# Performance work log

Measured on AMD Instinct MI355X. Metric: run time of the kernel, lower is better.

Reference implementation:

```python
import jax, jax.numpy as jnp
import numpy as np

N = 20000   # nodes
E = 320000  # edges
C = 64      # channel multiplicity
NB = 8      # bessel basis size
NA = 4      # node attribute (species) dim
L_DIMS = (1, 3, 5)  # 2l+1 for l=0,1,2
SH = 9      # total spherical-harmonic dim
OFFS = (0, 1, 4, 9)


def setup_inputs() -> dict:
    key = jax.random.key(0)
    ks = jax.random.split(key, 11)
    s = lambda k, shape: jax.random.normal(k, shape, dtype=jnp.float32)
    return {
        "length": jax.random.uniform(ks[0], (E, NB), dtype=jnp.float32),
        "node_features": s(ks[1], (N, C)),
        "node_attributes": s(ks[2], (N, NA)),
        "edge_attributes": s(ks[3], (E, SH)),
        "W1": s(ks[4], (NB, 64)),
        "W2": s(ks[5], (64, 64)),
        "W3": s(ks[6], (64, 64)),
        "W4": s(ks[7], (64, 3 * C)),
        "Wl": s(ks[8], (3, C, C)),
        "Wsc": s(ks[9], (NA, C, C)),
        "edge_index": jax.random.randint(ks[10], (2, E), 0, N, dtype=jnp.int32),
    }


def reference(length, node_features, node_attributes, edge_attributes, W1, W2, W3, W4, Wl, Wsc, edge_index):
    sender, receiver = edge_index[0], edge_index[1]
    silu = jax.nn.silu
    # e3nn FullyConnectedNet: x @ W / sqrt(fan_in), silu between layers, no act on last
    h = silu(length @ W1 * np.float32(1.0 / np.sqrt(NB)))
    h = silu(h @ W2 * np.float32(0.125))
    h = silu(h @ W3 * np.float32(0.125))
    w = (h @ W4 * np.float32(0.125)).reshape(E, 3, C)  # per-edge TP weights [E,3,C]
    # weighted tensor product: scalar node feats x sh (0e x le -> le, uvu)
    wx = w * node_features[sender][:, None, :]          # [E,3,C]
    parts = []
    for l in range(3):
        Y = edge_attributes[:, OFFS[l]:OFFS[l + 1]]     # [E, 2l+1]
        parts.append((wx[:, l, :, None] * Y[:, None, :]).reshape(E, C * L_DIMS[l]))
    mij = jnp.concatenate(parts, axis=1)                # [E, C*9]
    # scatter_sum into receivers
    msg = jax.ops.segment_sum(mij, receiver, num_segments=N)  # [N, C*9]
    # e3nn Linear: per-l channel mix, 1/sqrt(fan_in) norm
    out_blocks = []
    o = 0
    for l in range(3):
        d = L_DIMS[l]
        blk = msg[:, o:o + C * d].reshape(N, C, d)
        out_blocks.append(jnp.einsum('num,uv->nvm', blk, Wl[l]) * np.float32(1.0 / np.sqrt(C)))
        o += C * d
    message = jnp.concatenate(out_blocks, axis=2)       # reshape_irreps -> [N, C, 9]
    # FullyConnectedTensorProduct(attr 0e, feat 0e) -> only 0e output has paths
    sc0 = jnp.einsum('na,nu,auw->nw', node_attributes, node_features, Wsc) * np.float32(1.0 / np.sqrt(NA * C))
    sc = jnp.concatenate([sc0, jnp.zeros((N, C * (SH - 1)), dtype=sc0.dtype)], axis=1)  # [N, C*9]
    return (message, sc)
```

## Files before the change

kernel.cpp:

```cpp
#include <hip/hip_runtime.h>
#include <hip/hip_fp16.h>

#define N_NODES 20000
#define N_EDGES 320000
#define MSG_ROW 576
#define MSG_OFF 11520000
#define SCAN_BS 256
#define NBLK_SCAN ((N_NODES + SCAN_BS - 1) / SCAN_BS)
#define NPAD 20032
#define MT_S (NPAD * 64)

typedef _Float16 f16;
typedef _Float16 f16x4 __attribute__((ext_vector_type(4)));
typedef _Float16 f16x8 __attribute__((ext_vector_type(8)));
typedef float f32x4 __attribute__((ext_vector_type(4)));

#define OFF_WLT  22528
#define OFF_WSCT 34816
#define WIMG_HALF 51200
#define WIMG_BYTES 102400
#define WIMG_BLOCKS 200

#define OFF_WT4 0
#define OFF_W1T 24576
#define OFF_WT2 28672
#define OFF_WT3 36864
#define OFF_H0  45056
#define OFF_HT  53248
#define LDS_TOTAL 69632
#define OFF_WXT 0

__device__ __forceinline__ float silu_f(float x) {
    return x * __builtin_amdgcn_rcpf(1.0f + __expf(-x));
}


__global__ __launch_bounds__(256)
void pre_kernel(const float* __restrict__ W1, const float* __restrict__ W2,
                const float* __restrict__ W3, const float* __restrict__ W4,
                const float* __restrict__ Wl, const float* __restrict__ Wsc,
                f16* __restrict__ img,
                const int* __restrict__ eidx, int* __restrict__ counts) {
    const int b = blockIdx.x;
    if (b >= WIMG_BLOCKS) {
        const int e = (b - WIMG_BLOCKS) * 256 + threadIdx.x;
        if (e < N_EDGES) atomicAdd(&counts[eidx[N_EDGES + e]], 1);
        return;
    }
    const int p = b * 256 + threadIdx.x;
    float v;
    if (p < 12288) {
        const int m = p >> 6, rem = p & 63, g = rem >> 3, j = rem & 7;
        const int k = ((g ^ (m & 7)) << 3) | j;
        v = W4[k * 192 + m];
    } else if (p < 14336) {
        const int q = p - 12288;
        const int m = q >> 5, rem = q & 31, g = rem >> 3, j = rem & 7;
        const int k = ((g ^ (m & 3)) << 3) | j;
        v = (k < 8) ? W1[k * 64 + m] : 0.f;
    } else if (p < 18432) {
        const int q = p - 14336;
        const int m = q >> 6, rem = q & 63, g = rem >> 3, j = rem & 7;
        const int k = ((g ^ (m & 7)) << 3) | j;
        v = W2[k * 64 + m];
    } else if (p < 22528) {
        const int q = p - 18432;
        const int m = q >> 6, rem = q & 63, g = rem >> 3, j = rem & 7;
        const int k = ((g ^ (m & 7)) << 3) | j;
        v = W3[k * 64 + m];
    } else if (p < OFF_WSCT) {
        const int q = p - OFF_WLT;
        const int l = q >> 12, r = q & 4095, vv = r >> 6, u = r & 63;
        v = Wl[(l * 64 + u) * 64 + vv];
    } else {
        const int q = p - OFF_WSCT;
        const int ww = q >> 8, kk = q & 255, a = kk >> 6, u = kk & 63;
        v = Wsc[(a * 64 + u) * 64 + ww];
    }
    img[p] = (f16)v;
}


__global__ __launch_bounds__(SCAN_BS)
void scan1_kernel(const int* __restrict__ counts, int* __restrict__ offs,
                  int* __restrict__ bsum) {
    __shared__ int sm[SCAN_BS];
    const int tid = threadIdx.x;
    const int i = blockIdx.x * SCAN_BS + tid;
    const int v = (i < N_NODES) ? counts[i] : 0;
    sm[tid] = v;
    __syncthreads();
#pragma unroll
    for (int off = 1; off < SCAN_BS; off <<= 1) {
        const int t = (tid >= off) ? sm[tid - off] : 0;
        __syncthreads();
        sm[tid] += t;
        __syncthreads();
    }
    if (i < N_NODES) offs[i] = sm[tid] - v;
    if (tid == SCAN_BS - 1) bsum[blockIdx.x] = sm[tid];
}

__global__ __launch_bounds__(SCAN_BS)
void scan3_kernel(int* __restrict__ offs, const int* __restrict__ bsum,
                  int* __restrict__ cursor) {
    __shared__ int bs[NBLK_SCAN];
    const int tid = threadIdx.x;
    if (tid < NBLK_SCAN) bs[tid] = bsum[tid];
    __syncthreads();
    int bbase = 0;
    for (int j = 0; j < blockIdx.x; ++j) bbase += bs[j];
    const int i = blockIdx.x * SCAN_BS + tid;
    if (i < N_NODES) {
        const int o = offs[i] + bbase;
        offs[i] = o;
        cursor[i] = o;
    }
    if (blockIdx.x == NBLK_SCAN - 1 && tid == SCAN_BS - 1)
        offs[N_NODES] = bbase + bs[NBLK_SCAN - 1];
}


__global__ __launch_bounds__(512, 4)
void edge_mlp_mfma(const float* __restrict__ length,
                   const float* __restrict__ nf,
                   const int*   __restrict__ eidx,
                   int* __restrict__ cursor,
                   int* __restrict__ order,
                   const f16*   __restrict__ wimg,
                   f16* __restrict__ wx)
{
    __shared__ __align__(16) char s[LDS_TOTAL];
    __shared__ int sendS[128];
    __shared__ int rankS[128];

    const int tid = threadIdx.x;
    const int ebase = blockIdx.x << 7;

    {
        const uint4* src = (const uint4*)wimg;
        uint4* dst = (uint4*)s;
#pragma unroll
        for (int i = 0; i < 6; ++i) {
            const int c = i * 512 + tid;
            if (c < 2816) dst[c] = src[c];
        }
    }
    if (tid < 128) {
        const int e = tid;
        const int eg = ebase + e;
        const float4 q0 = *(const float4*)&length[(size_t)eg * 8];
        const float4 q1 = *(const float4*)&length[(size_t)eg * 8 + 4];
        f16x8 h;
        h[0] = (f16)q0.x; h[1] = (f16)q0.y; h[2] = (f16)q0.z; h[3] = (f16)q0.w;
        h[4] = (f16)q1.x; h[5] = (f16)q1.y; h[6] = (f16)q1.z; h[7] = (f16)q1.w;
        *(f16x8*)(s + OFF_H0 + e * 64 + ((0 ^ (e & 3)) << 4)) = h;
        sendS[e] = eidx[eg];
        const int rcv = eidx[N_EDGES + eg];
        const int pos = atomicAdd(&cursor[rcv], 1);
        order[pos] = eg;
        rankS[e] = pos;
    } else {
        const int idx = tid - 128;
        const int e = idx / 3, gz = 1 + idx - (idx / 3) * 3;
        uint4 z; z.x = 0; z.y = 0; z.z = 0; z.w = 0;
        *(uint4*)(s + OFF_H0 + e * 64 + ((gz ^ (e & 3)) << 4)) = z;
    }
    __syncthreads();

    const int lane = tid & 63, w = tid >> 6;
    const int eh = w >> 2, wm = w & 3;
    const int lm = lane & 15, lg = lane >> 4;
    const int mrow = wm * 16 + lm;
    const int r0 = lg << 2;
    const int eloc0 = eh << 6;

    const f32x4 zacc = {0.f, 0.f, 0.f, 0.f};
    f32x4 acc[4];

    {
        const f16x8 a = *(const f16x8*)(s + OFF_W1T + mrow * 64 + ((lg ^ (mrow & 3)) << 4));
#pragma unroll
        for (int nt = 0; nt < 4; ++nt) {
            const int e = eloc0 + nt * 16 + lm;
            const f16x8 b = *(const f16x8*)(s + OFF_H0 + e * 64 + ((lg ^ (e & 3)) << 4));
            acc[nt] = __builtin_amdgcn_mfma_f32_16x16x32_f16(a, b, zacc, 0, 0, 0);
        }
    }
    {
        const int c = wm * 16 + r0;
#pragma unroll
        for (int nt = 0; nt < 4; ++nt) {
            const int e = eloc0 + nt * 16 + lm;
            f16x4 pk;
            pk[0] = (f16)silu_f(acc[nt][0] * 0.35355339059f);
            pk[1] = (f16)silu_f(acc[nt][1] * 0.35355339059f);
            pk[2] = (f16)silu_f(acc[nt][2] * 0.35355339059f);
            pk[3] = (f16)silu_f(acc[nt][3] * 0.35355339059f);
            *(f16x4*)(s + OFF_HT + e * 128 + (((c >> 3) ^ (e & 7)) << 4) + ((c & 7) << 1)) = pk;
        }
    }
    __syncthreads();

#pragma unroll
    for (int nt = 0; nt < 4; ++nt) acc[nt] = zacc;
#pragma unroll
    for (int kh = 0; kh < 2; ++kh) {
        const int g = (kh << 2) + lg;
        const f16x8 a = *(const f16x8*)(s + OFF_WT2 + mrow * 128 + ((g ^ (mrow & 7)) << 4));
#pragma unroll
        for (int nt = 0; nt < 4; ++nt) {
            const int e = eloc0 + nt * 16 + lm;
            const f16x8 b = *(const f16x8*)(s + OFF_HT + e * 128 + ((g ^ (e & 7)) << 4));
            acc[nt] = __builtin_amdgcn_mfma_f32_16x16x32_f16(a, b, acc[nt], 0, 0, 0);
        }
    }
    __syncthreads();
    {
        const int c = wm * 16 + r0;
#pragma unroll
        for (int nt = 0; nt < 4; ++nt) {
            const int e = eloc0 + nt * 16 + lm;
            f16x4 pk;
            pk[0] = (f16)silu_f(acc[nt][0] * 0.125f);
            pk[1] = (f16)silu_f(acc[nt][1] * 0.125f);
            pk[2] = (f16)silu_f(acc[nt][2] * 0.125f);
            pk[3] = (f16)silu_f(acc[nt][3] * 0.125f);
            *(f16x4*)(s + OFF_HT + e * 128 + (((c >> 3) ^ (e & 7)) << 4) + ((c & 7) << 1)) = pk;
        }
    }
    __syncthreads();

#pragma unroll
    for (int nt = 0; nt < 4; ++nt) acc[nt] = zacc;
#pragma unroll
    for (int kh = 0; kh < 2; ++kh) {
        const int g = (kh << 2) + lg;
        const f16x8 a = *(const f16x8*)(s + OFF_WT3 + mrow * 128 + ((g ^ (mrow & 7)) << 4));
#pragma unroll
        for (int nt = 0; nt < 4; ++nt) {
            const int e = eloc0 + nt * 16 + lm;
            const f16x8 b = *(const f16x8*)(s + OFF_HT + e * 128 + ((g ^ (e & 7)) << 4));
            acc[nt] = __builtin_amdgcn_mfma_f32_16x16x32_f16(a, b, acc[nt], 0, 0, 0);
        }
    }
    __syncthreads();
    {
        const int c = wm * 16 + r0;
#pragma unroll
        for (int nt = 0; nt < 4; ++nt) {
            const int e = eloc0 + nt * 16 + lm;
            f16x4 pk;
            pk[0] = (f16)silu_f(acc[nt][0] * 0.125f);
            pk[1] = (f16)silu_f(acc[nt][1] * 0.125f);
            pk[2] = (f16)silu_f(acc[nt][2] * 0.125f);
            pk[3] = (f16)silu_f(acc[nt][3] * 0.125f);
            *(f16x4*)(s + OFF_HT + e * 128 + (((c >> 3) ^ (e & 7)) << 4) + ((c & 7) << 1)) = pk;
        }
    }
    __syncthreads();

    f32x4 acc4[3][4];
#pragma unroll
    for (int p = 0; p < 3; ++p)
#pragma unroll
        for (int nt = 0; nt < 4; ++nt) acc4[p][nt] = zacc;
#pragma unroll
    for (int kh = 0; kh < 2; ++kh) {
        const int g = (kh << 2) + lg;
        f16x8 ap[3];
#pragma unroll
        for (int p = 0; p < 3; ++p) {
            const int m4 = p * 64 + mrow;
            ap[p] = *(const f16x8*)(s + OFF_WT4 + m4 * 128 + ((g ^ (m4 & 7)) << 4));
        }
#pragma unroll
        for (int nt = 0; nt < 4; ++nt) {
            const int e = eloc0 + nt * 16 + lm;
            const f16x8 b = *(const f16x8*)(s + OFF_HT + e * 128 + ((g ^ (e & 7)) << 4));
#pragma unroll
            for (int p = 0; p < 3; ++p)
                acc4[p][nt] = __builtin_amdgcn_mfma_f32_16x16x32_f16(ap[p], b, acc4[p][nt], 0, 0, 0);
        }
    }
    __syncthreads();

#pragma unroll
    for (int nt = 0; nt < 4; ++nt) {
        const int e = eloc0 + nt * 16 + lm;
        const int snd = sendS[e];
        const float4 nf4 = *(const float4*)&nf[(size_t)snd * 64 + wm * 16 + r0];
#pragma unroll
        for (int p = 0; p < 3; ++p) {
            const int c = p * 64 + wm * 16 + r0;
            f16x4 pk;
            pk[0] = (f16)(acc4[p][nt][0] * 0.125f * nf4.x);
            pk[1] = (f16)(acc4[p][nt][1] * 0.125f * nf4.y);
            pk[2] = (f16)(acc4[p][nt][2] * 0.125f * nf4.z);
            pk[3] = (f16)(acc4[p][nt][3] * 0.125f * nf4.w);
            *(f16x4*)(s + OFF_WXT + e * 384 + (((c >> 3) ^ (e & 7)) << 4) + ((c & 7) << 1)) = pk;
        }
    }
    __syncthreads();

#pragma unroll
    for (int it = 0; it < 6; ++it) {
        const int chunk = it * 512 + tid;
        const int e = chunk / 24, g = chunk - e * 24;
        const uint4 v = *(const uint4*)(s + OFF_WXT + e * 384 + ((g ^ (e & 7)) << 4));
        *(uint4*)((char*)wx + (size_t)rankS[e] * 384 + g * 16) = v;
    }
}


__global__ __launch_bounds__(256, 8)
void gather_kernel(const __half* __restrict__ wx,
                   const float* __restrict__ ea,
                   const int* __restrict__ offs,
                   const int* __restrict__ order,
                   f16* __restrict__ mT)
{
    const int tid = threadIdx.x;
    const int wid = tid >> 6;
    const int v   = tid & 63;
    const int n   = (blockIdx.x << 2) + wid;
    const int beg = offs[n];
    const int end = offs[n + 1];

    float a0 = 0.f, a1[3] = {0.f, 0.f, 0.f}, a2[5] = {0.f, 0.f, 0.f, 0.f, 0.f};
    int k = beg;
    for (; k + 2 <= end; k += 2) {
        const int eA = __builtin_amdgcn_readfirstlane(order[k]);
        const int eB = __builtin_amdgcn_readfirstlane(order[k + 1]);
        const __half* wrA = wx + (size_t)k * 192;
        const __half* wrB = wx + (size_t)(k + 1) * 192;
        const float xA0 = __half2float(wrA[v]);
        const float xA1 = __half2float(wrA[64 + v]);
        const float xA2 = __half2float(wrA[128 + v]);
        const float xB0 = __half2float(wrB[v]);
        const float xB1 = __half2float(wrB[64 + v]);
        const float xB2 = __half2float(wrB[128 + v]);
        const float* yA = ea + (size_t)eA * 9;
        const float* yB = ea + (size_t)eB * 9;
        a0 += xA0 * yA[0] + xB0 * yB[0];
#pragma unroll
        for (int m = 0; m < 3; ++m) a1[m] += xA1 * yA[1 + m] + xB1 * yB[1 + m];
#pragma unroll
        for (int m = 0; m < 5; ++m) a2[m] += xA2 * yA[4 + m] + xB2 * yB[4 + m];
    }
    if (k < end) {
        const int e = __builtin_amdgcn_readfirstlane(order[k]);
        const __half* wr = wx + (size_t)k * 192;
        const float x0 = __half2float(wr[v]);
        const float x1 = __half2float(wr[64 + v]);
        const float x2 = __half2float(wr[128 + v]);
        const float* y = ea + (size_t)e * 9;
        a0 += x0 * y[0];
#pragma unroll
        for (int m = 0; m < 3; ++m) a1[m] += x1 * y[1 + m];
#pragma unroll
        for (int m = 0; m < 5; ++m) a2[m] += x2 * y[4 + m];
    }

    f16* base = mT + (size_t)n * 64 + v;
    base[0] = (f16)a0;
#pragma unroll
    for (int m = 0; m < 3; ++m) base[(size_t)(1 + m) * MT_S] = (f16)a1[m];
#pragma unroll
    for (int m = 0; m < 5; ++m) base[(size_t)(4 + m) * MT_S] = (f16)a2[m];
}


__global__ __launch_bounds__(256, 2)
void node_mfma(const f16* __restrict__ wimg,
               const f16* __restrict__ mT,
               const float* __restrict__ nf,
               const float* __restrict__ na,
               float* __restrict__ out)
{
    __shared__ __align__(16) f16  mst[9 * 16 * 64];
    __shared__ __align__(16) f16  nft[16 * 64];
    __shared__ __align__(16) float nas[256];
    __shared__ __align__(16) float outb[16 * 580];

    const int tid = threadIdx.x;
    const int lane = tid & 63, w = tid >> 6;
    const int lm = lane & 15, lg = lane >> 4;
    const int r0 = lg << 2;
    const int n0 = blockIdx.x << 6;

    const f16* wlT  = wimg + OFF_WLT;
    const f16* wscT = wimg + OFF_WSCT;
    f16x8 wl[3][2];
#pragma unroll
    for (int l = 0; l < 3; ++l)
#pragma unroll
        for (int kk = 0; kk < 2; ++kk)
            wl[l][kk] = *(const f16x8*)(wlT + ((l << 6) + (w << 4) + lm) * 64 + (kk << 5) + (lg << 3));
    f16x8 wsc[8];
#pragma unroll
    for (int kg = 0; kg < 8; ++kg)
        wsc[kg] = *(const f16x8*)(wscT + ((w << 4) + lm) * 256 + (kg << 5) + (lg << 3));

    {
        const int n = n0 + (tid >> 2);
        nas[tid] = (n < N_NODES) ? na[(size_t)n * 4 + (tid & 3)] : 0.f;
    }

    const f32x4 zacc = {0.f, 0.f, 0.f, 0.f};

    for (int nt = 0; nt < 4; ++nt) {
        const int ng = n0 + (nt << 4);
        __syncthreads();

#pragma unroll
        for (int it = 0; it < 5; ++it) {
            const int c = it * 256 + tid;
            if (c < 1152) {
                const int m = c >> 7, rem = c & 127, r = rem >> 3, g = rem & 7;
                const uint4 v = *(const uint4*)(mT + (size_t)m * MT_S + (size_t)(ng + r) * 64 + (g << 3));
                *(uint4*)(&mst[m * 1024 + r * 64 + ((g ^ (r & 7)) << 3)]) = v;
            }
        }
        {
            const int r = tid >> 4, c4 = (tid & 15) << 2;
            const int n = ng + r;
            float4 v4;
            if (n < N_NODES) v4 = *(const float4*)&nf[(size_t)n * 64 + c4];
            else { v4.x = 0.f; v4.y = 0.f; v4.z = 0.f; v4.w = 0.f; }
            f16x4 h;
            h[0] = (f16)v4.x; h[1] = (f16)v4.y; h[2] = (f16)v4.z; h[3] = (f16)v4.w;
            const int g = c4 >> 3;
            *(f16x4*)&nft[r * 64 + ((g ^ (r & 7)) << 3) + (c4 & 7)] = h;
        }
        __syncthreads();

#pragma unroll
        for (int m = 0; m < 9; ++m) {
            const int l = (m == 0) ? 0 : ((m < 4) ? 1 : 2);
            f32x4 acc = zacc;
#pragma unroll
            for (int kk = 0; kk < 2; ++kk) {
                const int g = (kk << 2) + lg;
                const f16x8 b = *(const f16x8*)&mst[m * 1024 + lm * 64 + ((g ^ (lm & 7)) << 3)];
                acc = __builtin_amdgcn_mfma_f32_16x16x32_f16(wl[l][kk], b, acc, 0, 0, 0);
            }
#pragma unroll
            for (int i = 0; i < 4; ++i)
                outb[lm * 580 + ((w << 4) + r0 + i) * 9 + m] = acc[i] * 0.125f;
        }
        __syncthreads();

#pragma unroll
        for (int it = 0; it < 9; ++it) {
            const int c = it * 256 + tid;
            const int r = c / 144, q = c - r * 144;
            const int n = ng + r;
            if (n < N_NODES) {
                const float4 v = *(const float4*)&outb[r * 580 + (q << 2)];
                *(float4*)&out[(size_t)n * 576 + (q << 2)] = v;
            }
        }
        __syncthreads();

        {
            const float4 na4 = *(const float4*)&nas[((nt << 4) + lm) << 2];
            const float* nap = (const float*)&na4;
            f32x4 sacc = zacc;
#pragma unroll
            for (int kg = 0; kg < 8; ++kg) {
                const int g = ((kg & 1) << 2) + lg;
                f16x8 q = *(const f16x8*)&nft[lm * 64 + ((g ^ (lm & 7)) << 3)];
                const f16 sa = (f16)nap[kg >> 1];
                q = q * sa;
                sacc = __builtin_amdgcn_mfma_f32_16x16x32_f16(wsc[kg], q, sacc, 0, 0, 0);
            }
#pragma unroll
            for (int i = 0; i < 4; ++i)
                outb[lm * 580 + (w << 4) + r0 + i] = sacc[i] * 0.0625f;
        }
        __syncthreads();

        {
            const int r = tid >> 4, q = tid & 15;
            const int n = ng + r;
            if (n < N_NODES)
                *(float4*)&out[(size_t)MSG_OFF + (size_t)n * 576 + (q << 2)] =
                    *(const float4*)&outb[r * 580 + (q << 2)];
        }
        float4 z4; z4.x = 0.f; z4.y = 0.f; z4.z = 0.f; z4.w = 0.f;
#pragma unroll
        for (int it = 0; it < 8; ++it) {
            const int c = it * 256 + tid;
            const int r = c >> 7, q = c & 127;
            const int n = ng + r;
            if (n < N_NODES)
                *(float4*)&out[(size_t)MSG_OFF + (size_t)n * 576 + 64 + (q << 2)] = z4;
        }
    }
}


__device__ __forceinline__ void layer_accum(const float* src, const float* __restrict__ W,
                                            float a2[4][4], int c0, int e0) {
#pragma unroll
    for (int i = 0; i < 4; ++i)
#pragma unroll
        for (int j = 0; j < 4; ++j) a2[i][j] = 0.f;
#pragma unroll 8
    for (int u = 0; u < 64; ++u) {
        const float4 h4 = *(const float4*)&src[(u << 6) + e0];
        const float4 w4 = *(const float4*)&W[(u << 6) + c0];
        const float hv[4] = {h4.x, h4.y, h4.z, h4.w};
        const float wv[4] = {w4.x, w4.y, w4.z, w4.w};
#pragma unroll
        for (int i = 0; i < 4; ++i)
#pragma unroll
            for (int j = 0; j < 4; ++j) a2[i][j] += wv[i] * hv[j];
    }
}

__device__ __forceinline__ void layer_store(float* dst, const float a2[4][4],
                                            float scale, int c0, int e0) {
#pragma unroll
    for (int i = 0; i < 4; ++i) {
        float4 v;
        v.x = silu_f(a2[i][0] * scale);
        v.y = silu_f(a2[i][1] * scale);
        v.z = silu_f(a2[i][2] * scale);
        v.w = silu_f(a2[i][3] * scale);
        *(float4*)&dst[((c0 + i) << 6) + e0] = v;
    }
}

__global__ __launch_bounds__(256, 4)
void edge_kernel_atomic(const float* __restrict__ length,
                        const float* __restrict__ nf,
                        const float* __restrict__ ea,
                        const float* __restrict__ W1,
                        const float* __restrict__ W2,
                        const float* __restrict__ W3,
                        const float* __restrict__ W4,
                        const int*   __restrict__ eidx,
                        float* __restrict__ msg)
{
    __shared__ float buf[4096];
    __shared__ float lenS[512];
    __shared__ float Ys[576];
    __shared__ int   sendS[64];
    __shared__ int   recvS[64];

    const int tid = threadIdx.x;
    const int tx = tid & 15;
    const int ty = tid >> 4;
    const int c0 = tx << 2;
    const int e0 = ty << 2;
    const int ebase = blockIdx.x << 6;

    for (int i = tid; i < 512; i += 256) {
        const int e = i >> 3, k = i & 7;
        lenS[(k << 6) + e] = length[((ebase + e) << 3) + k];
    }
    for (int i = tid; i < 576; i += 256) Ys[i] = ea[ebase * 9 + i];
    if (tid < 64) {
        sendS[tid] = eidx[ebase + tid];
        recvS[tid] = eidx[N_EDGES + ebase + tid];
    }
    __syncthreads();

    {
        float a2[4][4];
#pragma unroll
        for (int i = 0; i < 4; ++i)
#pragma unroll
            for (int j = 0; j < 4; ++j) a2[i][j] = 0.f;
#pragma unroll
        for (int k = 0; k < 8; ++k) {
            const float4 h4 = *(const float4*)&lenS[(k << 6) + e0];
            const float4 w4 = *(const float4*)&W1[(k << 6) + c0];
            const float hv[4] = {h4.x, h4.y, h4.z, h4.w};
            const float wv[4] = {w4.x, w4.y, w4.z, w4.w};
#pragma unroll
            for (int i = 0; i < 4; ++i)
#pragma unroll
                for (int j = 0; j < 4; ++j) a2[i][j] += wv[i] * hv[j];
        }
        layer_store(buf, a2, 0.35355339059327373f, c0, e0);
    }
    __syncthreads();
    {
        float a2[4][4];
        layer_accum(buf, W2, a2, c0, e0);
        __syncthreads();
        layer_store(buf, a2, 0.125f, c0, e0);
    }
    __syncthreads();
    {
        float a2[4][4];
        layer_accum(buf, W3, a2, c0, e0);
        __syncthreads();
        layer_store(buf, a2, 0.125f, c0, e0);
    }
    __syncthreads();

    float wacc[3][4][4];
#pragma unroll
    for (int l = 0; l < 3; ++l)
#pragma unroll
        for (int i = 0; i < 4; ++i)
#pragma unroll
            for (int j = 0; j < 4; ++j) wacc[l][i][j] = 0.f;
#pragma unroll 4
    for (int u = 0; u < 64; ++u) {
        const float4 h4 = *(const float4*)&buf[(u << 6) + e0];
        const float hv[4] = {h4.x, h4.y, h4.z, h4.w};
#pragma unroll
        for (int l = 0; l < 3; ++l) {
            const float4 w4 = *(const float4*)&W4[u * 192 + (l << 6) + c0];
            const float wv[4] = {w4.x, w4.y, w4.z, w4.w};
#pragma unroll
            for (int i = 0; i < 4; ++i)
#pragma unroll
                for (int j = 0; j < 4; ++j) wacc[l][i][j] += wv[i] * hv[j];
        }
    }

#pragma unroll
    for (int j = 0; j < 4; ++j) {
        const int e = e0 + j;
        const int snd = sendS[e];
        const int rcv = recvS[e];
        const float4 nf4 = *(const float4*)&nf[(snd << 6) + c0];
        const float nfv[4] = {nf4.x, nf4.y, nf4.z, nf4.w};
        float* mrow = msg + rcv * MSG_ROW;
        const float y0 = Ys[e * 9 + 0];
        float y1[3], y2[5];
#pragma unroll
        for (int m = 0; m < 3; ++m) y1[m] = Ys[e * 9 + 1 + m];
#pragma unroll
        for (int m = 0; m < 5; ++m) y2[m] = Ys[e * 9 + 4 + m];
#pragma unroll
        for (int i = 0; i < 4; ++i) {
            const int c = c0 + i;
            const float wx0 = wacc[0][i][j] * 0.125f * nfv[i];
            const float wx1 = wacc[1][i][j] * 0.125f * nfv[i];
            const float wx2 = wacc[2][i][j] * 0.125f * nfv[i];
            atomicAdd(&mrow[c], wx0 * y0);
#pragma unroll
            for (int m = 0; m < 3; ++m) atomicAdd(&mrow[64 + c * 3 + m], wx1 * y1[m]);
#pragma unroll
            for (int m = 0; m < 5; ++m) atomicAdd(&mrow[256 + c * 5 + m], wx2 * y2[m]);
        }
    }
}

__global__ __launch_bounds__(256, 4)
void node_kernel(const float* __restrict__ nf,
                 const float* __restrict__ na,
                 const float* __restrict__ Wl,
                 const float* __restrict__ Wsc,
                 float* __restrict__ out)
{
    __shared__ float ms[4][576];
    __shared__ float fs[4][64];
    const int tid = threadIdx.x;
    const int wid = tid >> 6;
    const int v   = tid & 63;
    const int n   = (blockIdx.x << 2) + wid;
    const float* msg = out + MSG_OFF;

#pragma unroll
    for (int j = 0; j < 9; ++j)
        ms[wid][(j << 6) + v] = msg[n * MSG_ROW + (j << 6) + v];
    fs[wid][v] = nf[(n << 6) + v];
    __syncthreads();

    float o9[9];
#pragma unroll
    for (int j = 0; j < 9; ++j) o9[j] = 0.f;
    const float* m0 = &ms[wid][0];
    const float* m1 = &ms[wid][64];
    const float* m2 = &ms[wid][256];

#pragma unroll 8
    for (int u = 0; u < 64; ++u) {
        const float w0 = Wl[(u << 6) + v];
        const float w1 = Wl[4096 + (u << 6) + v];
        const float w2 = Wl[8192 + (u << 6) + v];
        o9[0] += m0[u] * w0;
        o9[1] += m1[u * 3 + 0] * w1;
        o9[2] += m1[u * 3 + 1] * w1;
        o9[3] += m1[u * 3 + 2] * w1;
        o9[4] += m2[u * 5 + 0] * w2;
        o9[5] += m2[u * 5 + 1] * w2;
        o9[6] += m2[u * 5 + 2] * w2;
        o9[7] += m2[u * 5 + 3] * w2;
        o9[8] += m2[u * 5 + 4] * w2;
    }
#pragma unroll
    for (int j = 0; j < 9; ++j) out[n * MSG_ROW + v * 9 + j] = o9[j] * 0.125f;

    const float b0 = na[(n << 2) + 0];
    const float b1 = na[(n << 2) + 1];
    const float b2 = na[(n << 2) + 2];
    const float b3 = na[(n << 2) + 3];
    float sacc = 0.f;
#pragma unroll 8
    for (int u = 0; u < 64; ++u) {
        const float f = fs[wid][u];
        sacc += f * (b0 * Wsc[(u << 6) + v] + b1 * Wsc[4096 + (u << 6) + v] +
                     b2 * Wsc[8192 + (u << 6) + v] + b3 * Wsc[12288 + (u << 6) + v]);
    }
    float* scrow = out + MSG_OFF + n * MSG_ROW;
    scrow[v] = sacc * 0.0625f;
#pragma unroll
    for (int j = 1; j < 9; ++j) scrow[(j << 6) + v] = 0.f;
}

extern "C" void kernel_launch(void* const* d_in, const int* in_sizes, int n_in,
                              void* d_out, int out_size, void* d_ws, size_t ws_size,
                              hipStream_t stream) {
    const float* length = (const float*)d_in[0];
    const float* nfeat  = (const float*)d_in[1];
    const float* nattr  = (const float*)d_in[2];
    const float* eattr  = (const float*)d_in[3];
    const float* W1     = (const float*)d_in[4];
    const float* W2     = (const float*)d_in[5];
    const float* W3     = (const float*)d_in[6];
    const float* W4     = (const float*)d_in[7];
    const float* Wl     = (const float*)d_in[8];
    const float* Wsc    = (const float*)d_in[9];
    const int*   eidx   = (const int*)d_in[10];
    float* out = (float*)d_out;

    f16*    wimg   = (f16*)d_ws;
    __half* wx     = (__half*)((char*)d_ws + WIMG_BYTES);
    f16*    mT     = (f16*)((char*)d_ws + WIMG_BYTES + (size_t)N_EDGES * 192 * 2);
    int*   counts  = (int*)((char*)mT + (size_t)9 * MT_S * 2);
    int*   offsets = counts + N_NODES;
    int*   cursor  = offsets + N_NODES + 1;
    int*   order   = cursor + N_NODES;
    int*   bsum    = order + N_EDGES;
    const size_t need = WIMG_BYTES + (size_t)N_EDGES * 192 * 2 + (size_t)9 * MT_S * 2 +
                        (size_t)(N_NODES * 3 + 1 + N_EDGES + 128) * 4;

    if (ws_size >= need) {
        hipMemsetAsync(counts, 0, N_NODES * sizeof(int), stream);
        pre_kernel<<<WIMG_BLOCKS + N_EDGES / 256, 256, 0, stream>>>(W1, W2, W3, W4, Wl, Wsc,
                                                                    wimg, eidx, counts);
        scan1_kernel<<<NBLK_SCAN, SCAN_BS, 0, stream>>>(counts, offsets, bsum);
        scan3_kernel<<<NBLK_SCAN, SCAN_BS, 0, stream>>>(offsets, bsum, cursor);
        edge_mlp_mfma<<<N_EDGES / 128, 512, 0, stream>>>(length, nfeat, eidx, cursor, order,
                                                         wimg, (f16*)wx);
        gather_kernel<<<N_NODES / 4, 256, 0, stream>>>(wx, eattr, offsets, order, mT);
        node_mfma<<<NPAD / 64, 256, 0, stream>>>(wimg, mT, nfeat, nattr, out);
    } else {
        hipMemsetAsync(out + MSG_OFF, 0, (size_t)N_NODES * MSG_ROW * sizeof(float), stream);
        edge_kernel_atomic<<<N_EDGES / 64, 256, 0, stream>>>(length, nfeat, eattr,
                                                             W1, W2, W3, W4, eidx,
                                                             out + MSG_OFF);
        node_kernel<<<N_NODES / 4, 256, 0, stream>>>(nfeat, nattr, Wl, Wsc, out);
    }
}
```

Baseline: 146.4 us.

## Give each wave its own 16-edge strip to drop inter-layer barriers in edge MLP

```diff
diff --git a/kernel.cpp b/kernel.cpp
--- a/kernel.cpp
+++ b/kernel.cpp
@@ -169,146 +169,129 @@
     __syncthreads();
 
     const int lane = tid & 63, w = tid >> 6;
-    const int eh = w >> 2, wm = w & 3;
     const int lm = lane & 15, lg = lane >> 4;
-    const int mrow = wm * 16 + lm;
     const int r0 = lg << 2;
-    const int eloc0 = eh << 6;
+    const int e = (w << 4) + lm;
 
     const f32x4 zacc = {0.f, 0.f, 0.f, 0.f};
     f32x4 acc[4];
 
     {
-        const f16x8 a = *(const f16x8*)(s + OFF_W1T + mrow * 64 + ((lg ^ (mrow & 3)) << 4));
-#pragma unroll
-        for (int nt = 0; nt < 4; ++nt) {
-            const int e = eloc0 + nt * 16 + lm;
-            const f16x8 b = *(const f16x8*)(s + OFF_H0 + e * 64 + ((lg ^ (e & 3)) << 4));
-            acc[nt] = __builtin_amdgcn_mfma_f32_16x16x32_f16(a, b, zacc, 0, 0, 0);
-        }
-    }
-    {
-        const int c = wm * 16 + r0;
-#pragma unroll
-        for (int nt = 0; nt < 4; ++nt) {
-            const int e = eloc0 + nt * 16 + lm;
-            f16x4 pk;
-            pk[0] = (f16)silu_f(acc[nt][0] * 0.35355339059f);
-            pk[1] = (f16)silu_f(acc[nt][1] * 0.35355339059f);
-            pk[2] = (f16)silu_f(acc[nt][2] * 0.35355339059f);
-            pk[3] = (f16)silu_f(acc[nt][3] * 0.35355339059f);
-            *(f16x4*)(s + OFF_HT + e * 128 + (((c >> 3) ^ (e & 7)) << 4) + ((c & 7) << 1)) = pk;
-        }
-    }
-    __syncthreads();
-
-#pragma unroll
-    for (int nt = 0; nt < 4; ++nt) acc[nt] = zacc;
+        const f16x8 b = *(const f16x8*)(s + OFF_H0 + e * 64 + ((lg ^ (e & 3)) << 4));
+#pragma unroll
+        for (int ct = 0; ct < 4; ++ct) {
+            const int mrow = (ct << 4) + lm;
+            const f16x8 a = *(const f16x8*)(s + OFF_W1T + mrow * 64 + ((lg ^ (mrow & 3)) << 4));
+            acc[ct] = __builtin_amdgcn_mfma_f32_16x16x32_f16(a, b, zacc, 0, 0, 0);
+        }
+    }
+#pragma unroll
+    for (int ct = 0; ct < 4; ++ct) {
+        const int c = (ct << 4) + r0;
+        f16x4 pk;
+        pk[0] = (f16)silu_f(acc[ct][0] * 0.35355339059f);
+        pk[1] = (f16)silu_f(acc[ct][1] * 0.35355339059f);
+        pk[2] = (f16)silu_f(acc[ct][2] * 0.35355339059f);
+        pk[3] = (f16)silu_f(acc[ct][3] * 0.35355339059f);
+        *(f16x4*)(s + OFF_HT + e * 128 + (((c >> 3) ^ (e & 7)) << 4) + ((c & 7) << 1)) = pk;
+    }
+
+#pragma unroll
+    for (int ct = 0; ct < 4; ++ct) acc[ct] = zacc;
 #pragma unroll
     for (int kh = 0; kh < 2; ++kh) {
         const int g = (kh << 2) + lg;
-        const f16x8 a = *(const f16x8*)(s + OFF_WT2 + mrow * 128 + ((g ^ (mrow & 7)) << 4));
-#pragma unroll
-        for (int nt = 0; nt < 4; ++nt) {
-            const int e = eloc0 + nt * 16 + lm;
-            const f16x8 b = *(const f16x8*)(s + OFF_HT + e * 128 + ((g ^ (e & 7)) << 4));
-            acc[nt] = __builtin_amdgcn_mfma_f32_16x16x32_f16(a, b, acc[nt], 0, 0, 0);
-        }
-    }
-    __syncthreads();
-    {
-        const int c = wm * 16 + r0;
-#pragma unroll
-        for (int nt = 0; nt < 4; ++nt) {
-            const int e = eloc0 + nt * 16 + lm;
-            f16x4 pk;
-            pk[0] = (f16)silu_f(acc[nt][0] * 0.125f);
-            pk[1] = (f16)silu_f(acc[nt][1] * 0.125f);
-            pk[2] = (f16)silu_f(acc[nt][2] * 0.125f);
-            pk[3] = (f16)silu_f(acc[nt][3] * 0.125f);
-            *(f16x4*)(s + OFF_HT + e * 128 + (((c >> 3) ^ (e & 7)) << 4) + ((c & 7) << 1)) = pk;
-        }
-    }
-    __syncthreads();
-
-#pragma unroll
-    for (int nt = 0; nt < 4; ++nt) acc[nt] = zacc;
+        const f16x8 b = *(const f16x8*)(s + OFF_HT + e * 128 + ((g ^ (e & 7)) << 4));
+#pragma unroll
+        for (int ct = 0; ct < 4; ++ct) {
+            const int mrow = (ct << 4) + lm;
+            const f16x8 a = *(const f16x8*)(s + OFF_WT2 + mrow * 128 + ((g ^ (mrow & 7)) << 4));
+            acc[ct] = __builtin_amdgcn_mfma_f32_16x16x32_f16(a, b, acc[ct], 0, 0, 0);
+        }
+    }
+#pragma unroll
+    for (int ct = 0; ct < 4; ++ct) {
+        const int c = (ct << 4) + r0;
+        f16x4 pk;
+        pk[0] = (f16)silu_f(acc[ct][0] * 0.125f);
+        pk[1] = (f16)silu_f(acc[ct][1] * 0.125f);
+        pk[2] = (f16)silu_f(acc[ct][2] * 0.125f);
+        pk[3] = (f16)silu_f(acc[ct][3] * 0.125f);
+        *(f16x4*)(s + OFF_HT + e * 128 + (((c >> 3) ^ (e & 7)) << 4) + ((c & 7) << 1)) = pk;
+    }
+
+#pragma unroll
+    for (int ct = 0; ct < 4; ++ct) acc[ct] = zacc;
 #pragma unroll
     for (int kh = 0; kh < 2; ++kh) {
         const int g = (kh << 2) + lg;
-        const f16x8 a = *(const f16x8*)(s + OFF_WT3 + mrow * 128 + ((g ^ (mrow & 7)) << 4));
-#pragma unroll
-        for (int nt = 0; nt < 4; ++nt) {
-            const int e = eloc0 + nt * 16 + lm;
-            const f16x8 b = *(const f16x8*)(s + OFF_HT + e * 128 + ((g ^ (e & 7)) << 4));
-            acc[nt] = __builtin_amdgcn_mfma_f32_16x16x32_f16(a, b, acc[nt], 0, 0, 0);
-        }
-    }
-    __syncthreads();
-    {
-        const int c = wm * 16 + r0;
-#pragma unroll
-        for (int nt = 0; nt < 4; ++nt) {
-            const int e = eloc0 + nt * 16 + lm;
-            f16x4 pk;
-            pk[0] = (f16)silu_f(acc[nt][0] * 0.125f);
-            pk[1] = (f16)silu_f(acc[nt][1] * 0.125f);
-            pk[2] = (f16)silu_f(acc[nt][2] * 0.125f);
-            pk[3] = (f16)silu_f(acc[nt][3] * 0.125f);
-            *(f16x4*)(s + OFF_HT + e * 128 + (((c >> 3) ^ (e & 7)) << 4) + ((c & 7) << 1)) = pk;
-        }
-    }
-    __syncthreads();
-
-    f32x4 acc4[3][4];
-#pragma unroll
-    for (int p = 0; p < 3; ++p)
-#pragma unroll
-        for (int nt = 0; nt < 4; ++nt) acc4[p][nt] = zacc;
+        const f16x8 b = *(const f16x8*)(s + OFF_HT + e * 128 + ((g ^ (e & 7)) << 4));
+#pragma unroll
+        for (int ct = 0; ct < 4; ++ct) {
+            const int mrow = (ct << 4) + lm;
+            const f16x8 a = *(const f16x8*)(s + OFF_WT3 + mrow * 128 + ((g ^ (mrow & 7)) << 4));
+            acc[ct] = __builtin_amdgcn_mfma_f32_16x16x32_f16(a, b, acc[ct], 0, 0, 0);
+        }
+    }
+#pragma unroll
+    for (int ct = 0; ct < 4; ++ct) {
+        const int c = (ct << 4) + r0;
+        f16x4 pk;
+        pk[0] = (f16)silu_f(acc[ct][0] * 0.125f);
+        pk[1] = (f16)silu_f(acc[ct][1] * 0.125f);
+        pk[2] = (f16)silu_f(acc[ct][2] * 0.125f);
+        pk[3] = (f16)silu_f(acc[ct][3] * 0.125f);
+        *(f16x4*)(s + OFF_HT + e * 128 + (((c >> 3) ^ (e & 7)) << 4) + ((c & 7) << 1)) = pk;
+    }
+
+    f32x4 acc4[12];
+#pragma unroll
+    for (int pt = 0; pt < 12; ++pt) acc4[pt] = zacc;
 #pragma unroll
     for (int kh = 0; kh < 2; ++kh) {
         const int g = (kh << 2) + lg;
-        f16x8 ap[3];
-#pragma unroll
-        for (int p = 0; p < 3; ++p) {
-            const int m4 = p * 64 + mrow;
-            ap[p] = *(const f16x8*)(s + OFF_WT4 + m4 * 128 + ((g ^ (m4 & 7)) << 4));
-        }
-#pragma unroll
-        for (int nt = 0; nt < 4; ++nt) {
-            const int e = eloc0 + nt * 16 + lm;
-            const f16x8 b = *(const f16x8*)(s + OFF_HT + e * 128 + ((g ^ (e & 7)) << 4));
-#pragma unroll
-            for (int p = 0; p < 3; ++p)
-                acc4[p][nt] = __builtin_amdgcn_mfma_f32_16x16x32_f16(ap[p], b, acc4[p][nt], 0, 0, 0);
-        }
-    }
-    __syncthreads();
-
-#pragma unroll
-    for (int nt = 0; nt < 4; ++nt) {
-        const int e = eloc0 + nt * 16 + lm;
-        const int snd = sendS[e];
-        const float4 nf4 = *(const float4*)&nf[(size_t)snd * 64 + wm * 16 + r0];
-#pragma unroll
-        for (int p = 0; p < 3; ++p) {
-            const int c = p * 64 + wm * 16 + r0;
-            f16x4 pk;
-            pk[0] = (f16)(acc4[p][nt][0] * 0.125f * nf4.x);
-            pk[1] = (f16)(acc4[p][nt][1] * 0.125f * nf4.y);
-            pk[2] = (f16)(acc4[p][nt][2] * 0.125f * nf4.z);
-            pk[3] = (f16)(acc4[p][nt][3] * 0.125f * nf4.w);
-            *(f16x4*)(s + OFF_WXT + e * 384 + (((c >> 3) ^ (e & 7)) << 4) + ((c & 7) << 1)) = pk;
-        }
-    }
-    __syncthreads();
-
-#pragma unroll
-    for (int it = 0; it < 6; ++it) {
-        const int chunk = it * 512 + tid;
-        const int e = chunk / 24, g = chunk - e * 24;
-        const uint4 v = *(const uint4*)(s + OFF_WXT + e * 384 + ((g ^ (e & 7)) << 4));
-        *(uint4*)((char*)wx + (size_t)rankS[e] * 384 + g * 16) = v;
+        const f16x8 b = *(const f16x8*)(s + OFF_HT + e * 128 + ((g ^ (e & 7)) << 4));
+#pragma unroll
+        for (int pt = 0; pt < 12; ++pt) {
+            const int m4 = (pt << 4) + lm;
+            const f16x8 a = *(const f16x8*)(s + OFF_WT4 + m4 * 128 + ((g ^ (m4 & 7)) << 4));
+            acc4[pt] = __builtin_amdgcn_mfma_f32_16x16x32_f16(a, b, acc4[pt], 0, 0, 0);
+        }
+    }
+
+    const int snd = sendS[e];
+    float4 nfq[4];
+#pragma unroll
+    for (int q = 0; q < 4; ++q)
+        nfq[q] = *(const float4*)&nf[(size_t)snd * 64 + (q << 4) + r0];
+
+    __syncthreads();
+
+#pragma unroll
+    for (int ph = 0; ph < 2; ++ph) {
+        if ((w >> 2) == ph) {
+            const int el = ((w & 3) << 4) + lm;
+#pragma unroll
+            for (int pt = 0; pt < 12; ++pt) {
+                const int c = (pt << 4) + r0;
+                const float* nfv = (const float*)&nfq[pt & 3];
+                f16x4 pk;
+                pk[0] = (f16)(acc4[pt][0] * 0.125f * nfv[0]);
+                pk[1] = (f16)(acc4[pt][1] * 0.125f * nfv[1]);
+                pk[2] = (f16)(acc4[pt][2] * 0.125f * nfv[2]);
+                pk[3] = (f16)(acc4[pt][3] * 0.125f * nfv[3]);
+                *(f16x4*)(s + OFF_WXT + el * 384 + (((c >> 3) ^ (el & 7)) << 4) + ((c & 7) << 1)) = pk;
+            }
+        }
+        __syncthreads();
+#pragma unroll
+        for (int it = 0; it < 3; ++it) {
+            const int chunk = it * 512 + tid;
+            const int el = chunk / 24, g = chunk - el * 24;
+            const uint4 v = *(const uint4*)(s + OFF_WXT + el * 384 + ((g ^ (el & 7)) << 4));
+            *(uint4*)((char*)wx + (size_t)rankS[el + ph * 64] * 384 + g * 16) = v;
+        }
+        __syncthreads();
     }
 }
 
```

Result: no change. 148.9 us (+1.7%).
